# Kernel tuning notes

Hardware: AMD Instinct MI355X
Metric: run time of the kernel (lower is better)

## Reference

```python
import jax, jax.numpy as jnp
import numpy as np

D_MODEL = 1024
NUM_HEAD = 16
D_HEAD = 64


def setup_inputs() -> dict:
    key = jax.random.key(0)
    ks = jax.random.split(key, 9)
    b, p = 8, 1024
    s = 1.0 / np.sqrt(D_MODEL)
    inp = {
        "x": jax.random.normal(ks[0], (b, p, D_MODEL), jnp.float32),
        "w_q": jax.random.uniform(ks[1], (D_MODEL, D_MODEL), jnp.float32, -s, s),
        "b_q": jax.random.uniform(ks[2], (D_MODEL,), jnp.float32, -s, s),
        "w_k": jax.random.uniform(ks[3], (D_MODEL, D_MODEL), jnp.float32, -s, s),
        "b_k": jax.random.uniform(ks[4], (D_MODEL,), jnp.float32, -s, s),
        "w_v": jax.random.uniform(ks[5], (D_MODEL, D_MODEL), jnp.float32, -s, s),
        "b_v": jax.random.uniform(ks[6], (D_MODEL,), jnp.float32, -s, s),
        "w_o": jax.random.uniform(ks[7], (D_MODEL, D_MODEL), jnp.float32, -s, s),
        "b_o": jax.random.uniform(ks[8], (D_MODEL,), jnp.float32, -s, s),
    }
    return inp


def reference(x, w_q, b_q, w_k, b_k, w_v, b_v, w_o, b_o):
    b, p, _ = x.shape
    # projections (torch Linear: y = x @ W.T + b; here weights stored [in,out])
    q = x @ w_q + b_q
    k = x @ w_k + b_k
    v = x @ w_v + b_v
    # [b, h, p, d]
    q = q.reshape(b, p, NUM_HEAD, D_HEAD).transpose(0, 2, 1, 3)
    k = k.reshape(b, p, NUM_HEAD, D_HEAD).transpose(0, 2, 1, 3)
    v = v.reshape(b, p, NUM_HEAD, D_HEAD).transpose(0, 2, 1, 3)
    scale = 1.0 / np.sqrt(D_HEAD).astype(np.float32)
    scores = jnp.einsum("bhqd,bhkd->bhqk", q, k) * scale
    attn = jax.nn.softmax(scores, axis=-1)
    out = jnp.einsum("bhqk,bhkd->bhqd", attn, v)
    out = out.transpose(0, 2, 1, 3).reshape(b, p, D_MODEL)
    return out @ w_o + b_o
```

## Files before the change

### kernel.cpp

```cpp
#include <hip/hip_runtime.h>
#include <stdint.h>


typedef __attribute__((ext_vector_type(8))) short short8;
typedef __attribute__((ext_vector_type(4))) short s16x4;
typedef __attribute__((ext_vector_type(4))) float f32x4;

__device__ __forceinline__ short f2bf(float f) {
  unsigned u = __builtin_bit_cast(unsigned, f);
  u += 0x7fffu + ((u >> 16) & 1u);
  return (short)(u >> 16);
}

__device__ __forceinline__ unsigned pk2bf(float a, float b) {
  unsigned ua = __builtin_bit_cast(unsigned, a);
  unsigned ub = __builtin_bit_cast(unsigned, b);
  ua += 0x7fffu + ((ua >> 16) & 1u);
  ub += 0x7fffu + ((ub >> 16) & 1u);
  return (ua >> 16) | (ub & 0xffff0000u);
}

__device__ __forceinline__ unsigned cvtpk(float a, float b) {
  unsigned r;
  asm("v_cvt_pk_bf16_f32 %0, %1, %2" : "=v"(r) : "v"(a), "v"(b));
  return r;
}

__device__ __forceinline__ float fexp2(float x) {
  float r;
  asm("v_exp_f32 %0, %1" : "=v"(r) : "v"(x));
  return r;
}

typedef __attribute__((address_space(3))) void lds_void;
typedef __attribute__((address_space(1))) void gbl_void;
#define GLD16(gp, lp) \
  __builtin_amdgcn_global_load_lds((gbl_void*)(gp), (lds_void*)(lp), 16, 0, 0)

#define MFMA(a, b, c) __builtin_amdgcn_mfma_f32_16x16x32_bf16((a), (b), (c), 0, 0, 0)

__global__ __launch_bounds__(256) void k_prep(const float* __restrict__ x,
                                              short* __restrict__ xb,
                                              const float* __restrict__ s0,
                                              const float* __restrict__ s1,
                                              const float* __restrict__ s2,
                                              const float* __restrict__ s3,
                                              short* __restrict__ d0,
                                              short* __restrict__ d1,
                                              short* __restrict__ d2,
                                              short* __restrict__ d3) {
  if (blockIdx.z == 4) {
    int t = threadIdx.y * 32 + threadIdx.x;
    int bid = blockIdx.y * 32 + blockIdx.x;
#pragma unroll
    for (int j = 0; j < 4; ++j) {
      int i = (bid * 1024 + j * 256 + t) * 8;
      const float4* s = (const float4*)(x + i);
      float4 f0 = s[0], f1 = s[1];
      short8 o;
      o[0] = f2bf(f0.x); o[1] = f2bf(f0.y); o[2] = f2bf(f0.z); o[3] = f2bf(f0.w);
      o[4] = f2bf(f1.x); o[5] = f2bf(f1.y); o[6] = f2bf(f1.z); o[7] = f2bf(f1.w);
      *(short8*)(xb + i) = o;
    }
    return;
  }
  __shared__ float tile[32][33];
  const float* srcs[4] = {s0, s1, s2, s3};
  short* dsts[4] = {d0, d1, d2, d3};
  const float* src = srcs[blockIdx.z];
  short* dst = dsts[blockIdx.z];
  int tx = threadIdx.x, ty = threadIdx.y;
  int x0 = blockIdx.x * 32, y0 = blockIdx.y * 32;
#pragma unroll
  for (int i = 0; i < 32; i += 8)
    tile[ty + i][tx] = src[(y0 + ty + i) * 1024 + x0 + tx];
  __syncthreads();
#pragma unroll
  for (int i = 0; i < 32; i += 8)
    dst[(x0 + ty + i) * 1024 + y0 + tx] = f2bf(tile[tx][ty + i]);
}

template <int MODE>
__global__ __launch_bounds__(256, 3) void k_gemm(const short* __restrict__ A,
                                                 const short* __restrict__ Bt,
                                                 const float* __restrict__ bias0,
                                                 const float* __restrict__ bias1,
                                                 const float* __restrict__ bias2,
                                                 short* __restrict__ o0,
                                                 short* __restrict__ o1,
                                                 short* __restrict__ o2,
                                                 float* __restrict__ of) {
  __shared__ __align__(16) short a_lds[128 * 64];
  __shared__ __align__(16) short b_lds[128 * 64];
  const int tid = threadIdx.x;
  const int l = blockIdx.x;
  const int m0 = ((((l & 7) << 3) | ((l >> 3) & 7))) << 7;
  const int n0 = (l >> 6) << 7;
  const int w = tid >> 6;
  const int lane = tid & 63;
  const int ll = lane & 15;
  const int qd = lane >> 4;
  const int wm = (w & 1) * 64;
  const int wn = (w >> 1) * 64;

  const int srow = tid >> 3;
  const int schunk = ((tid & 7) ^ (srow & 7)) * 8;
  const short* ag = A + (long)(m0 + srow) * 1024 + schunk;
  const short* bg = Bt + (long)(n0 + srow) * 1024 + schunk;

  f32x4 acc[4][4] = {};

  for (int kt = 0; kt < 1024; kt += 64) {
#pragma unroll
    for (int j = 0; j < 4; ++j) {
      GLD16(ag + j * 32768 + kt, &a_lds[j * 2048 + tid * 8]);
      GLD16(bg + j * 32768 + kt, &b_lds[j * 2048 + tid * 8]);
    }
    __syncthreads();
#pragma unroll
    for (int kh = 0; kh < 2; ++kh) {
      const int xoff = (((kh * 4 + qd) ^ (ll & 7)) * 8);
      short8 af[4], bfr[4];
#pragma unroll
      for (int mt = 0; mt < 4; ++mt)
        af[mt] = *(const short8*)&a_lds[(wm + mt * 16 + ll) * 64 + xoff];
#pragma unroll
      for (int nt = 0; nt < 4; ++nt)
        bfr[nt] = *(const short8*)&b_lds[(wn + nt * 16 + ll) * 64 + xoff];
#pragma unroll
      for (int mt = 0; mt < 4; ++mt)
#pragma unroll
        for (int nt = 0; nt < 4; ++nt)
          acc[mt][nt] = MFMA(af[mt], bfr[nt], acc[mt][nt]);
    }
    __syncthreads();
  }

  if (MODE == 0) {
#pragma unroll
    for (int nt = 0; nt < 4; ++nt) {
      int n = n0 + wn + nt * 16 + ll;
      int which = n >> 10;
      int nl = n & 1023;
      int h = nl >> 6, d = n & 63;
      if (which == 2) {
        float bv = bias2[nl];
        const int b = m0 >> 10;
        const int p0 = (m0 & 1023) + wm;
#pragma unroll
        for (int mt = 0; mt < 4; ++mt) {
          int p = p0 + mt * 16 + qd * 4;
          int2 pk;
          pk.x = (int)pk2bf(acc[mt][nt][0] + bv, acc[mt][nt][1] + bv);
          pk.y = (int)pk2bf(acc[mt][nt][2] + bv, acc[mt][nt][3] + bv);
          *(int2*)&o2[(long)(b * 16 + h) * 65536 + d * 1024 + p] = pk;
        }
      } else {
        float bv = (which == 0) ? bias0[nl] : bias1[nl];
        float sc = (which == 0) ? 0.18033688f : 1.0f;
        short* o = (which == 0) ? o0 : o1;
#pragma unroll
        for (int mt = 0; mt < 4; ++mt) {
#pragma unroll
          for (int r = 0; r < 4; ++r) {
            int m = m0 + wm + mt * 16 + qd * 4 + r;
            int b = m >> 10, p = m & 1023;
            o[(long)(b * 16 + h) * 65536 + p * 64 + d] = f2bf((acc[mt][nt][r] + bv) * sc);
          }
        }
      }
    }
  } else {
#pragma unroll
    for (int nt = 0; nt < 4; ++nt) {
      int n = n0 + wn + nt * 16 + ll;
      float bv = bias0[n];
#pragma unroll
      for (int mt = 0; mt < 4; ++mt) {
#pragma unroll
        for (int r = 0; r < 4; ++r) {
          int m = m0 + wm + mt * 16 + qd * 4 + r;
          of[(long)m * 1024 + n] = acc[mt][nt][r] + bv;
        }
      }
    }
  }
}

__global__ __launch_bounds__(256, 4) void k_attn(const short* __restrict__ Q,
                                                 const short* __restrict__ K,
                                                 const short* __restrict__ VT,
                                                 short* __restrict__ O) {
  __shared__ __align__(16) short k_lds[2][4096];
  __shared__ __align__(16) short vt_lds[2][4096];
  const int tid = threadIdx.x;
  const int w = tid >> 6, lane = tid & 63, ll = lane & 15, qd = lane >> 4;
  const int bid = blockIdx.x;
  const int xcd = bid & 7;
  const int inner = bid >> 3;
  const int bh = xcd * 16 + (inner & 15);
  const int qb = inner >> 4;
  const long hoff = (long)bh * 65536;
  const int qr0 = qb * 128 + w * 32;

  const short* qg = Q + hoff + (long)(qr0 + ll) * 64 + qd * 8;
  short8 qf[2][2];
  qf[0][0] = *(const short8*)qg;
  qf[0][1] = *(const short8*)(qg + 32);
  qf[1][0] = *(const short8*)(qg + 1024);
  qf[1][1] = *(const short8*)(qg + 1024 + 32);

  const int sr = tid >> 3;
  const int swz = (tid & 7) ^ (sr & 7);
  const int pr = (sr & 0x23) | ((sr & 0x0C) << 1) | ((sr & 0x10) >> 2);
  const short* kg = K + hoff + pr * 64 + swz * 8;
  const short* vg = VT + hoff + (long)sr * 1024 + swz * 8;

  const int swzr = ll & 7;
  const int fro0 = ll * 64 + ((qd ^ swzr) * 8);
  const int fro1 = ll * 64 + (((4 + qd) ^ swzr) * 8);

  f32x4 oacc[2][4] = {};
  float l_part[2] = {0.f, 0.f};

  GLD16(kg, &k_lds[0][tid * 8]);
  GLD16(kg + 2048, &k_lds[0][2048 + tid * 8]);
  GLD16(vg, &vt_lds[0][tid * 8]);
  GLD16(vg + 32768, &vt_lds[0][2048 + tid * 8]);
  __syncthreads();

#pragma unroll 2
  for (int c = 0; c < 16; ++c) {
    const int cur = c & 1, nxt = cur ^ 1;
    if (c < 15) {
      GLD16(kg + (c + 1) * 4096, &k_lds[nxt][tid * 8]);
      GLD16(kg + (c + 1) * 4096 + 2048, &k_lds[nxt][2048 + tid * 8]);
      GLD16(vg + (c + 1) * 64, &vt_lds[nxt][tid * 8]);
      GLD16(vg + (c + 1) * 64 + 32768, &vt_lds[nxt][2048 + tid * 8]);
    }

    f32x4 s[2][4];
    __builtin_amdgcn_s_setprio(1);
#pragma unroll
    for (int jt = 0; jt < 4; ++jt) {
      short8 kf0 = *(const short8*)&k_lds[cur][jt * 1024 + fro0];
      short8 kf1 = *(const short8*)&k_lds[cur][jt * 1024 + fro1];
      f32x4 t0 = {};
      t0 = MFMA(kf0, qf[0][0], t0);
      t0 = MFMA(kf1, qf[0][1], t0);
      s[0][jt] = t0;
      f32x4 t1 = {};
      t1 = MFMA(kf0, qf[1][0], t1);
      t1 = MFMA(kf1, qf[1][1], t1);
      s[1][jt] = t1;
    }
    __builtin_amdgcn_s_setprio(0);

    short8 pf[2][2];
#pragma unroll
    for (int g = 0; g < 2; ++g) {
      float rs = 0.f;
#pragma unroll
      for (int jt = 0; jt < 4; ++jt)
#pragma unroll
        for (int r = 0; r < 4; ++r) {
          float e = fexp2(s[g][jt][r]);
          s[g][jt][r] = e;
          rs += e;
        }
      l_part[g] += rs;
#pragma unroll
      for (int u = 0; u < 2; ++u) {
        union { short8 v; unsigned x[4]; } pk;
        pk.x[0] = cvtpk(s[g][2 * u][0], s[g][2 * u][1]);
        pk.x[1] = cvtpk(s[g][2 * u][2], s[g][2 * u][3]);
        pk.x[2] = cvtpk(s[g][2 * u + 1][0], s[g][2 * u + 1][1]);
        pk.x[3] = cvtpk(s[g][2 * u + 1][2], s[g][2 * u + 1][3]);
        pf[g][u] = pk.v;
      }
    }

    __builtin_amdgcn_s_setprio(1);
#pragma unroll
    for (int dt = 0; dt < 4; ++dt) {
      short8 vf0 = *(const short8*)&vt_lds[cur][dt * 1024 + fro0];
      short8 vf1 = *(const short8*)&vt_lds[cur][dt * 1024 + fro1];
      oacc[0][dt] = MFMA(vf0, pf[0][0], oacc[0][dt]);
      oacc[0][dt] = MFMA(vf1, pf[0][1], oacc[0][dt]);
      oacc[1][dt] = MFMA(vf0, pf[1][0], oacc[1][dt]);
      oacc[1][dt] = MFMA(vf1, pf[1][1], oacc[1][dt]);
    }
    __builtin_amdgcn_s_setprio(0);
    __syncthreads();
  }

  const int b = bh >> 4, h = bh & 15;
#pragma unroll
  for (int g = 0; g < 2; ++g) {
    float l = l_part[g];
    l += __shfl_xor(l, 16, 64);
    l += __shfl_xor(l, 32, 64);
    const float inv = 1.0f / l;
    const long row = (long)(b * 1024 + qr0 + g * 16 + ll);
#pragma unroll
    for (int dt = 0; dt < 4; ++dt) {
      int2 ov;
      ov.x = (int)cvtpk(oacc[g][dt][0] * inv, oacc[g][dt][1] * inv);
      ov.y = (int)cvtpk(oacc[g][dt][2] * inv, oacc[g][dt][3] * inv);
      *(int2*)&O[row * 1024 + h * 64 + dt * 16 + qd * 4] = ov;
    }
  }
}

extern "C" void kernel_launch(void* const* d_in, const int* in_sizes, int n_in,
                              void* d_out, int out_size, void* d_ws, size_t ws_size,
                              hipStream_t stream) {
  const float* x   = (const float*)d_in[0];
  const float* w_q = (const float*)d_in[1];
  const float* b_q = (const float*)d_in[2];
  const float* w_k = (const float*)d_in[3];
  const float* b_k = (const float*)d_in[4];
  const float* w_v = (const float*)d_in[5];
  const float* b_v = (const float*)d_in[6];
  const float* w_o = (const float*)d_in[7];
  const float* b_o = (const float*)d_in[8];

  char* ws = (char*)d_ws;
  short* xb    = (short*)(ws);
  short* wqkvT = (short*)(ws + (16ull << 20));
  short* woT   = (short*)(ws + (22ull << 20));
  short* qw    = (short*)(ws + (24ull << 20));
  short* kw    = (short*)(ws + (40ull << 20));
  short* vw    = (short*)(ws + (56ull << 20));

  k_prep<<<dim3(32, 32, 5), dim3(32, 8), 0, stream>>>(
      x, xb, w_q, w_k, w_v, w_o,
      wqkvT, wqkvT + (1 << 20), wqkvT + (2 << 20), woT);

  k_gemm<0><<<1536, 256, 0, stream>>>(xb, wqkvT, b_q, b_k, b_v,
                                      qw, kw, vw, nullptr);

  k_attn<<<dim3(1024), 256, 0, stream>>>(qw, kw, vw, xb);

  k_gemm<1><<<512, 256, 0, stream>>>(xb, woT, b_o, nullptr, nullptr,
                                     nullptr, nullptr, nullptr, (float*)d_out);
}
```

Measured before the change: 231.9 us.

## Replace QKV GEMM with 256x256-tile, 4-stage pipelined 512-thread kernel

Adds a dedicated QKV projection kernel that uses 256x256 output tiles, 512 threads (8 waves, each computing 128x64), and a four-buffer LDS ring with async global-to-LDS loads issued three tiles ahead and explicit vmcnt waits. MFMA blocks are wrapped in setprio to favor math issue. The goal is more data reuse per LDS load and better overlap of memory with compute than the previous 128x128 single-buffered kernel. The grid drops to 384 blocks, which may leave CUs unevenly loaded and raises register and LDS pressure.

Result: slower. 241.6 us (+4.2%).

```diff
diff --git a/kernel.cpp b/kernel.cpp
--- a/kernel.cpp
+++ b/kernel.cpp
@@ -78,6 +78,120 @@
 #pragma unroll
   for (int i = 0; i < 32; i += 8)
     dst[(x0 + ty + i) * 1024 + y0 + tx] = f2bf(tile[tx][ty + i]);
+}
+
+__global__ __launch_bounds__(512, 2) void k_gemm_qkv(const short* __restrict__ A,
+                                                     const short* __restrict__ Bt,
+                                                     const float* __restrict__ bias0,
+                                                     const float* __restrict__ bias1,
+                                                     const float* __restrict__ bias2,
+                                                     short* __restrict__ o0,
+                                                     short* __restrict__ o1,
+                                                     short* __restrict__ o2) {
+  __shared__ __align__(16) short a_lds[4][256 * 32];
+  __shared__ __align__(16) short b_lds[4][256 * 32];
+  const int tid = threadIdx.x;
+  const int l = blockIdx.x;
+  const int li = l >> 3;
+  const int m0 = ((l & 7) * 4 + (li & 3)) << 8;
+  const int n0 = (li >> 2) << 8;
+
+  const int lane = tid & 63;
+  const int ll = lane & 15;
+  const int qd = lane >> 4;
+  const int wm = (tid >> 8) * 128;
+  const int wn = ((tid >> 6) & 3) * 64;
+
+  const int srow = tid >> 2;
+  const int gc = (tid & 3) ^ ((srow >> 1) & 3);
+  const short* ag = A + (long)(m0 + srow) * 1024 + gc * 8;
+  const short* bg = Bt + (long)(n0 + srow) * 1024 + gc * 8;
+
+  const int xsl = (qd ^ ((ll >> 1) & 3)) * 8;
+
+  f32x4 acc[8][4] = {};
+
+#define STAGE(t)                                              \
+  {                                                           \
+    const int _b = (t) & 3;                                   \
+    const int _k = (t) * 32;                                  \
+    GLD16(ag + _k, &a_lds[_b][tid * 8]);                      \
+    GLD16(ag + 131072 + _k, &a_lds[_b][4096 + tid * 8]);      \
+    GLD16(bg + _k, &b_lds[_b][tid * 8]);                      \
+    GLD16(bg + 131072 + _k, &b_lds[_b][4096 + tid * 8]);      \
+  }
+
+#define TILE(kt, VM, PF)                                                     \
+  {                                                                          \
+    asm volatile("s_waitcnt vmcnt(" #VM ")" ::: "memory");                   \
+    __builtin_amdgcn_s_barrier();                                            \
+    if (PF) STAGE((kt) + 3);                                                 \
+    short8 af[8], bf8[4];                                                    \
+    _Pragma("unroll")                                                        \
+    for (int mi = 0; mi < 8; ++mi)                                           \
+      af[mi] = *(const short8*)&a_lds[(kt) & 3][(wm + mi * 16 + ll) * 32 + xsl]; \
+    _Pragma("unroll")                                                        \
+    for (int ni = 0; ni < 4; ++ni)                                           \
+      bf8[ni] = *(const short8*)&b_lds[(kt) & 3][(wn + ni * 16 + ll) * 32 + xsl]; \
+    __builtin_amdgcn_s_setprio(1);                                           \
+    _Pragma("unroll")                                                        \
+    for (int mi = 0; mi < 8; ++mi)                                           \
+      _Pragma("unroll")                                                      \
+      for (int ni = 0; ni < 4; ++ni)                                         \
+        acc[mi][ni] = MFMA(af[mi], bf8[ni], acc[mi][ni]);                    \
+    __builtin_amdgcn_s_setprio(0);                                           \
+  }
+
+  STAGE(0); STAGE(1); STAGE(2);
+
+#pragma unroll 4
+  for (int kt = 0; kt < 28; ++kt) TILE(kt, 8, 1)
+  TILE(28, 8, 1)
+  TILE(29, 8, 0)
+  TILE(30, 4, 0)
+  TILE(31, 0, 0)
+
+#undef TILE
+#undef STAGE
+
+  const int which = n0 >> 10;
+  const int nb = n0 & 1023;
+  if (which == 2) {
+    const int b = m0 >> 10;
+    const int p0 = (m0 & 1023) + wm;
+#pragma unroll
+    for (int ni = 0; ni < 4; ++ni) {
+      int nl = nb + wn + ni * 16 + ll;
+      float bv = bias2[nl];
+      int h = nl >> 6, d = nl & 63;
+#pragma unroll
+      for (int mi = 0; mi < 8; ++mi) {
+        int p = p0 + mi * 16 + qd * 4;
+        int2 pk;
+        pk.x = (int)pk2bf(acc[mi][ni][0] + bv, acc[mi][ni][1] + bv);
+        pk.y = (int)pk2bf(acc[mi][ni][2] + bv, acc[mi][ni][3] + bv);
+        *(int2*)&o2[(long)(b * 16 + h) * 65536 + d * 1024 + p] = pk;
+      }
+    }
+  } else {
+    const float* bias = which ? bias1 : bias0;
+    short* o = which ? o1 : o0;
+    const float sc = which ? 1.0f : 0.18033688f;
+#pragma unroll
+    for (int ni = 0; ni < 4; ++ni) {
+      int nl = nb + wn + ni * 16 + ll;
+      float bv = bias[nl];
+      int h = nl >> 6, d = nl & 63;
+#pragma unroll
+      for (int mi = 0; mi < 8; ++mi)
+#pragma unroll
+        for (int r = 0; r < 4; ++r) {
+          int m = m0 + wm + mi * 16 + qd * 4 + r;
+          int b = m >> 10, p = m & 1023;
+          o[(long)(b * 16 + h) * 65536 + p * 64 + d] = f2bf((acc[mi][ni][r] + bv) * sc);
+        }
+    }
+  }
 }
 
 template <int MODE>
@@ -137,39 +251,6 @@
   }
 
   if (MODE == 0) {
-#pragma unroll
-    for (int nt = 0; nt < 4; ++nt) {
-      int n = n0 + wn + nt * 16 + ll;
-      int which = n >> 10;
-      int nl = n & 1023;
-      int h = nl >> 6, d = n & 63;
-      if (which == 2) {
-        float bv = bias2[nl];
-        const int b = m0 >> 10;
-        const int p0 = (m0 & 1023) + wm;
-#pragma unroll
-        for (int mt = 0; mt < 4; ++mt) {
-          int p = p0 + mt * 16 + qd * 4;
-          int2 pk;
-          pk.x = (int)pk2bf(acc[mt][nt][0] + bv, acc[mt][nt][1] + bv);
-          pk.y = (int)pk2bf(acc[mt][nt][2] + bv, acc[mt][nt][3] + bv);
-          *(int2*)&o2[(long)(b * 16 + h) * 65536 + d * 1024 + p] = pk;
-        }
-      } else {
-        float bv = (which == 0) ? bias0[nl] : bias1[nl];
-        float sc = (which == 0) ? 0.18033688f : 1.0f;
-        short* o = (which == 0) ? o0 : o1;
-#pragma unroll
-        for (int mt = 0; mt < 4; ++mt) {
-#pragma unroll
-          for (int r = 0; r < 4; ++r) {
-            int m = m0 + wm + mt * 16 + qd * 4 + r;
-            int b = m >> 10, p = m & 1023;
-            o[(long)(b * 16 + h) * 65536 + p * 64 + d] = f2bf((acc[mt][nt][r] + bv) * sc);
-          }
-        }
-      }
-    }
   } else {
 #pragma unroll
     for (int nt = 0; nt < 4; ++nt) {
@@ -337,8 +418,7 @@
       x, xb, w_q, w_k, w_v, w_o,
       wqkvT, wqkvT + (1 << 20), wqkvT + (2 << 20), woT);
 
-  k_gemm<0><<<1536, 256, 0, stream>>>(xb, wqkvT, b_q, b_k, b_v,
-                                      qw, kw, vw, nullptr);
+  k_gemm_qkv<<<384, 512, 0, stream>>>(xb, wqkvT, b_q, b_k, b_v, qw, kw, vw);
 
   k_attn<<<dim3(1024), 256, 0, stream>>>(qw, kw, vw, xb);
 
```
